# Optimization experiments

Measured on AMD Instinct MI355X. Metric: run time of the kernel, lower is better.

Reference implementation:

```python
import jax, jax.numpy as jnp
import numpy as np

N, F, H, K, E = 50000, 64, 64, 16, 800000
EXPONENT = 1.0  # module default; s = softmax(logits)**exponent, renormalized
EPS = 1e-15


def gcn_conv(x, W, b, src, dst, ew, n):
    """GCNConv: X' = D^{-1/2}(A+I)D^{-1/2} X W + b (symmetric norm, self-loops)."""
    h = x @ W  # [N,H] linear before propagation
    idx = jnp.arange(n)
    src_a = jnp.concatenate([src, idx])
    dst_a = jnp.concatenate([dst, idx])
    w_a = jnp.concatenate([ew, jnp.ones((n,), h.dtype)])
    deg = jax.ops.segment_sum(w_a, dst_a, num_segments=n)
    dinv = jnp.where(deg > 0, jax.lax.rsqrt(deg), 0.0)
    norm = dinv[src_a] * w_a * dinv[dst_a]          # [E+N]
    out = jax.ops.segment_sum(norm[:, None] * h[src_a], dst_a, num_segments=n)
    return out + b


def setup_inputs() -> dict:
    key = jax.random.key(0)
    ks = jax.random.split(key, 10)
    x = jax.random.normal(ks[0], (N, F), dtype=jnp.float32)
    edge_index = jax.random.randint(ks[1], (2, E), 0, N, dtype=jnp.int64)
    edge_weight = jax.random.uniform(ks[2], (E,), dtype=jnp.float32)
    W1 = jax.random.normal(ks[3], (F, H), dtype=jnp.float32) * (1.0 / np.sqrt(F))
    b1 = jnp.zeros((H,), jnp.float32)
    W2 = jax.random.normal(ks[4], (H, H), dtype=jnp.float32) * (1.0 / np.sqrt(H))
    b2 = jnp.zeros((H,), jnp.float32)
    Wp = jax.random.normal(ks[5], (H, K), dtype=jnp.float32) * (1.0 / np.sqrt(H))
    bp = jnp.zeros((K,), jnp.float32)
    return {"x": x, "edge_index": edge_index, "edge_weight": edge_weight,
            "W1": W1, "b1": b1, "W2": W2, "b2": b2, "Wp": Wp, "bp": bp}


def reference(x, edge_index, edge_weight, W1, b1, W2, b2, Wp, bp):
    src, dst = edge_index[0], edge_index[1]
    n = x.shape[0]
    k = Wp.shape[1]
    # stacked GCN + SELU
    h = jax.nn.selu(gcn_conv(x, W1, b1, src, dst, edge_weight, n))
    h = jax.nn.selu(gcn_conv(h, W2, b2, src, dst, edge_weight, n))
    # DMoN soft assignment
    s = jax.nn.softmax(h @ Wp + bp, axis=-1)          # [N,K]
    s = s ** EXPONENT
    s = s / s.sum(-1, keepdims=True)
    # pooled features: SELU(S^T X)
    out = jax.nn.selu(s.T @ h)                        # [K,H]
    # pooled adjacency: S^T A S computed over the edge list
    out_adj = jnp.einsum('ek,ec->kc', s[src] * edge_weight[:, None], s[dst])
    # spectral (modularity) loss
    d = jax.ops.segment_sum(edge_weight, src, num_segments=n)  # degrees
    two_m = edge_weight.sum()
    ca = s.T @ d                                      # [K]
    spectral_loss = -(jnp.trace(out_adj) - (ca @ ca) / two_m) / two_m
    # orthogonality loss
    ss = s.T @ s
    i_k = jnp.eye(k, dtype=s.dtype)
    ortho_loss = jnp.linalg.norm(ss / jnp.linalg.norm(ss) - i_k / jnp.sqrt(jnp.float32(k)))
    # cluster-size loss
    cluster_loss = jnp.linalg.norm(s.sum(0)) / n * jnp.sqrt(jnp.float32(k)) - 1.0
    # post-process pooled adjacency: zero diag, symmetric degree normalization
    adj = out_adj * (1.0 - i_k)
    dd = jnp.sqrt(adj.sum(-1))[:, None] + EPS
    adj = adj / dd / dd.T
    return s[None], out[None], adj[None], spectral_loss, ortho_loss, cluster_loss
```

## Files before the change

kernel.cpp:

```cpp
#include <hip/hip_runtime.h>
#include <hip/hip_bf16.h>

typedef __hip_bfloat16 bf16;
typedef long long i64t;

__device__ __forceinline__ float b2f(bf16 x) { return __bfloat162float(x); }
__device__ __forceinline__ bf16 f2b(float x) { return __float2bfloat16(x); }

__device__ __forceinline__ float loadF(const void* p, int isbf, long long i) {
    return isbf ? b2f(((const bf16*)p)[i]) : ((const float*)p)[i];
}
__device__ __forceinline__ int loadI(const void* p, int is64, long long i) {
    return is64 ? (int)((const i64t*)p)[i] : ((const int*)p)[i];
}
__device__ __forceinline__ void storeO(void* p, int isbf, long long i, float v) {
    if (isbf) ((bf16*)p)[i] = f2b(v);
    else ((float*)p)[i] = v;
}

#define SELU_ALPHA 1.6732632423543772f
#define SELU_SCALE 1.0507009873554805f
__device__ __forceinline__ float selu_f(float x) {
    return SELU_SCALE * (x > 0.f ? x : SELU_ALPHA * (expf(x) - 1.f));
}

__device__ __forceinline__ void atomAddF(float* p, float v) { unsafeAtomicAdd(p, v); }

__device__ __forceinline__ int pk_src(unsigned p) { return (int)(p >> 16); }
__device__ __forceinline__ float pk_w(unsigned p) { return __uint_as_float(p << 16); }

#define RED_STY 0
#define RED_OADJ 1024
#define RED_SS 1280
#define RED_CA 1536
#define RED_CS 1552
#define RED_2M 1568

#define NB_OADJ 1024
#define NB_ST 1024

#define CH 2048
#define NBK 256
#define BW 256

__global__ void k_probe(const void* W1, const void* eidx, int* flags) {
    __shared__ int sc[2];
    if (threadIdx.x == 0) { sc[0] = 0; sc[1] = 0; }
    __syncthreads();
    const unsigned* w = (const unsigned*)W1;
    int c0 = 0;
    for (int i = threadIdx.x; i < 2048; i += 256) {
        unsigned lo = w[i] & 0xFFFFu;
        unsigned e = (lo >> 7) & 0xFFu;
        if (e == 0u || (e >= 0x60u && e <= 0x8Fu)) c0++;
    }
    const unsigned* iw = (const unsigned*)eidx;
    int c1 = 0;
    for (int i = threadIdx.x; i < 2048; i += 256)
        if (iw[2 * i + 1] == 0u) c1++;
    atomicAdd(&sc[0], c0);
    atomicAdd(&sc[1], c1);
    __syncthreads();
    if (threadIdx.x == 0) {
        flags[0] = sc[0] > 1200 ? 1 : 0;
        flags[1] = sc[1] > 1024 ? 1 : 0;
    }
}

__global__ void k_bhist(const void* __restrict__ eidx, const int* __restrict__ flags,
                        int* __restrict__ gbcnt, int E) {
    __shared__ int cnt[NBK];
    int t = threadIdx.x;
    cnt[t] = 0;
    __syncthreads();
    int fi = flags[1];
    int base = blockIdx.x * CH;
    int m = min(CH, E - base);
    for (int k = t; k < m; k += 256) {
        int d = loadI(eidx, fi, (long long)E + base + k);
        atomicAdd(&cnt[d >> 8], 1);
    }
    __syncthreads();
    if (cnt[t]) atomicAdd(&gbcnt[t], cnt[t]);
}

__global__ void k_scanB(const int* __restrict__ gbcnt, int* __restrict__ gofs,
                        int* __restrict__ bbase) {
    __shared__ int part[NBK];
    int t = threadIdx.x;
    int c = gbcnt[t];
    part[t] = c;
    __syncthreads();
    for (int off = 1; off < NBK; off <<= 1) {
        int v = (t >= off) ? part[t - off] : 0;
        __syncthreads();
        part[t] += v;
        __syncthreads();
    }
    int ex = t ? part[t - 1] : 0;
    bbase[t] = ex;
    gofs[t] = ex;
    if (t == NBK - 1) bbase[NBK] = part[NBK - 1];
}

__global__ void k_bscatter(const void* __restrict__ eidx, const void* __restrict__ ew,
                           const int* __restrict__ flags, int* __restrict__ gofs,
                           uint2* __restrict__ tmp, int E) {
    __shared__ int cnt[NBK];
    __shared__ int binStart[NBK];
    __shared__ int bofs[NBK];
    __shared__ int runBase[NBK];
    __shared__ int sc[NBK];
    __shared__ uint2 staged[CH];
    int t = threadIdx.x;
    cnt[t] = 0;
    __syncthreads();
    int fb = flags[0], fi = flags[1];
    int base = blockIdx.x * CH;
    int m = min(CH, E - base);
    unsigned es[8], ed[8];
#pragma unroll
    for (int u = 0; u < 8; u++) {
        int k = t + u * 256;
        if (k < m) {
            int s = loadI(eidx, fi, base + k);
            int d = loadI(eidx, fi, (long long)E + base + k);
            float w = loadF(ew, fb, base + k);
            unsigned wb = (__float_as_uint(w) + 0x8000u) >> 16;
            es[u] = ((unsigned)s << 16) | wb;
            ed[u] = (unsigned)d;
            atomicAdd(&cnt[d >> 8], 1);
        } else {
            ed[u] = 0xFFFFFFFFu;
        }
    }
    __syncthreads();
    sc[t] = cnt[t];
    __syncthreads();
    for (int off = 1; off < NBK; off <<= 1) {
        int v = (t >= off) ? sc[t - off] : 0;
        __syncthreads();
        sc[t] += v;
        __syncthreads();
    }
    int ex = t ? sc[t - 1] : 0;
    binStart[t] = ex;
    bofs[t] = ex;
    __syncthreads();
#pragma unroll
    for (int u = 0; u < 8; u++) {
        if (ed[u] != 0xFFFFFFFFu) {
            int b = (int)(ed[u] >> 8);
            int li = atomicAdd(&bofs[b], 1);
            staged[li] = make_uint2(es[u], ed[u]);
        }
    }
    int c = cnt[t];
    __syncthreads();
    runBase[t] = c ? atomicAdd(&gofs[t], c) : 0;
    __syncthreads();
    for (int i = t; i < m; i += 256) {
        uint2 e = staged[i];
        int b = (int)(e.y >> 8);
        tmp[(long long)runBase[b] + (i - binStart[b])] = e;
    }
}

__global__ void k_build(const uint2* __restrict__ tmp, const int* __restrict__ bbase,
                        int* __restrict__ rowptr, unsigned* __restrict__ srcW,
                        float* __restrict__ dinv, float* __restrict__ two_m,
                        int n, int E) {
    __shared__ int cnt[BW];
    __shared__ int nofs[BW];
    __shared__ float wsum[BW];
    __shared__ int inc[BW];
    int b = blockIdx.x;
    int t = threadIdx.x;
    int n0 = b << 8;
    int nn = min(BW, n - n0);
    cnt[t] = 0;
    wsum[t] = 0.f;
    __syncthreads();
    int lo = bbase[b], hi = bbase[b + 1];
    for (int i = lo + t; i < hi; i += 256) {
        uint2 e = tmp[i];
        int dlo = (int)e.y - n0;
        atomicAdd(&cnt[dlo], 1);
        atomicAdd(&wsum[dlo], pk_w(e.x));
    }
    __syncthreads();
    inc[t] = cnt[t];
    __syncthreads();
    for (int off = 1; off < BW; off <<= 1) {
        int v = (t >= off) ? inc[t - off] : 0;
        __syncthreads();
        inc[t] += v;
        __syncthreads();
    }
    if (t < nn) {
        int ex = t ? inc[t - 1] : 0;
        rowptr[n0 + t] = lo + ex;
        nofs[t] = lo + ex;
        dinv[n0 + t] = rsqrtf(wsum[t] + 1.f);
    }
    if (b == (int)gridDim.x - 1 && t == 0) rowptr[n] = E;
    {
        float v = (t < nn) ? wsum[t] : 0.f;
        __shared__ float part[4];
        for (int mm = 32; mm; mm >>= 1) v += __shfl_down(v, mm, 64);
        int wid = t >> 6, lane = t & 63;
        if (lane == 0) part[wid] = v;
        __syncthreads();
        if (t == 0) atomAddF(two_m, part[0] + part[1] + part[2] + part[3]);
    }
    __syncthreads();
    for (int i = lo + t; i < hi; i += 256) {
        uint2 e = tmp[i];
        int dlo = (int)e.y - n0;
        int pos = atomicAdd(&nofs[dlo], 1);
        srcW[pos] = e.x;
    }
}

__global__ void k_gemm64(const void* __restrict__ in, int in_tag,
                         const void* __restrict__ W, const int* __restrict__ flags,
                         bf16* __restrict__ out, int n) {
    __shared__ float Wl[4096];
    __shared__ float Rl[2048];
    int t = threadIdx.x;
    int fb = flags[0];
    int inbf = in_tag ? fb : 0;
    for (int idx = t; idx < 4096; idx += 256) Wl[idx] = loadF(W, fb, idx);
    int r0 = blockIdx.x * 32;
    for (int idx = t; idx < 2048; idx += 256) {
        int rl = idx >> 6, k = idx & 63;
        int r = r0 + rl;
        Rl[idx] = (r < n) ? loadF(in, inbf, (long long)r * 64 + k) : 0.f;
    }
    __syncthreads();
    int rl = t >> 6, c = t & 63;
    float acc[8];
#pragma unroll
    for (int u = 0; u < 8; u++) acc[u] = 0.f;
    for (int k = 0; k < 64; k++) {
        float wv = Wl[k * 64 + c];
#pragma unroll
        for (int u = 0; u < 8; u++) acc[u] += Rl[(rl + (u << 2)) * 64 + k] * wv;
    }
#pragma unroll
    for (int u = 0; u < 8; u++) {
        int r = r0 + rl + (u << 2);
        if (r < n) out[(long long)r * 64 + c] = f2b(acc[u]);
    }
}

__global__ void k_prop_csr(const int* __restrict__ rowptr, const unsigned* __restrict__ srcW,
                           const float* __restrict__ dinv, const bf16* __restrict__ hin,
                           const void* __restrict__ b, const int* __restrict__ flags,
                           float* __restrict__ out, int n) {
    int t = threadIdx.x;
    int node = blockIdx.x * 4 + (t >> 6);
    if (node >= n) return;
    int l = t & 63;
    int q = l >> 4;
    int k = l & 15;
    int fb = flags[0];
    int i0 = rowptr[node], i1 = rowptr[node + 1];
    float di = dinv[node];
    float a0 = 0.f, a1 = 0.f, a2 = 0.f, a3 = 0.f;
    for (int base = i0; base < i1; base += 64) {
        int idx = base + l;
        unsigned p = (idx < i1) ? srcW[idx] : 0u;
        float cw = pk_w(p) * dinv[pk_src(p)];
        int m = i1 - base;
        if (m > 64) m = 64;
        for (int j = 0; j < m; j += 4) {
            unsigned pe = (unsigned)__shfl((int)p, j + q, 64);
            float c = __shfl(cw, j + q, 64);
            int s = (int)(pe >> 16);
            uint2 hv = *(const uint2*)(hin + ((long long)s << 6) + (k << 2));
            a0 += c * __uint_as_float(hv.x << 16);
            a1 += c * __uint_as_float(hv.x & 0xFFFF0000u);
            a2 += c * __uint_as_float(hv.y << 16);
            a3 += c * __uint_as_float(hv.y & 0xFFFF0000u);
        }
    }
    a0 += __shfl_xor(a0, 16, 64); a0 += __shfl_xor(a0, 32, 64);
    a1 += __shfl_xor(a1, 16, 64); a1 += __shfl_xor(a1, 32, 64);
    a2 += __shfl_xor(a2, 16, 64); a2 += __shfl_xor(a2, 32, 64);
    a3 += __shfl_xor(a3, 16, 64); a3 += __shfl_xor(a3, 32, 64);
    if (q == 0) {
        uint2 hv = *(const uint2*)(hin + ((long long)node << 6) + (k << 2));
        float dd = di * di;
        float v0 = di * a0 + dd * __uint_as_float(hv.x << 16) + loadF(b, fb, 4 * k);
        float v1 = di * a1 + dd * __uint_as_float(hv.x & 0xFFFF0000u) + loadF(b, fb, 4 * k + 1);
        float v2 = di * a2 + dd * __uint_as_float(hv.y << 16) + loadF(b, fb, 4 * k + 2);
        float v3 = di * a3 + dd * __uint_as_float(hv.y & 0xFFFF0000u) + loadF(b, fb, 4 * k + 3);
        float4 r = make_float4(selu_f(v0), selu_f(v1), selu_f(v2), selu_f(v3));
        *(float4*)(out + ((long long)node << 6) + (k << 2)) = r;
    }
}

__global__ void k_softmax(const float* __restrict__ y, const void* __restrict__ Wp,
                          const void* __restrict__ bp, const int* __restrict__ flags,
                          float* __restrict__ sbuf, void* __restrict__ sout, int n) {
    __shared__ float Wl[1024];
    __shared__ float bl[16];
    __shared__ float yl[1024];
    int t = threadIdx.x;
    int fb = flags[0];
    for (int idx = t; idx < 1024; idx += 256) Wl[idx] = loadF(Wp, fb, idx);
    if (t < 16) bl[t] = loadF(bp, fb, t);
    int g0 = blockIdx.x * 16;
    for (int idx = t; idx < 1024; idx += 256) {
        int nl = idx >> 6, f = idx & 63;
        int g = g0 + nl;
        yl[idx] = (g < n) ? y[(long long)g * 64 + f] : 0.f;
    }
    __syncthreads();
    int nl = t >> 4, k = t & 15;
    int g = g0 + nl;
    float logit = bl[k];
#pragma unroll
    for (int jj = 0; jj < 64; jj++) logit += yl[nl * 64 + jj] * Wl[jj * 16 + k];
    float mx = logit;
    for (int m = 8; m; m >>= 1) mx = fmaxf(mx, __shfl_xor(mx, m, 16));
    float e = expf(logit - mx);
    float sum = e;
    for (int m = 8; m; m >>= 1) sum += __shfl_xor(sum, m, 16);
    float sv = e / sum;
    if (g < n) {
        sbuf[(long long)g * 16 + k] = sv;
        storeO(sout, fb, (long long)g * 16 + k, sv);
    }
}

__global__ void k_stats(const float* __restrict__ s, const float* __restrict__ y,
                        float* __restrict__ scratch, int n) {
    __shared__ float lsty[1024];
    __shared__ float lss[256];
    int t = threadIdx.x;
    int w = t >> 6, f = t & 63;
    for (int i = t; i < 1024; i += 256) lsty[i] = 0.f;
    lss[t] = 0.f;
    __syncthreads();
    int chunk = (n + NB_ST - 1) / NB_ST;
    int start = min(blockIdx.x * chunk, n);
    int end = min(start + chunk, n);
    int q = (chunk + 3) >> 2;
    int n0 = min(start + w * q, end);
    int n1 = min(n0 + q, end);
    float acc[16], accss[16];
#pragma unroll
    for (int k = 0; k < 16; k++) { acc[k] = 0.f; accss[k] = 0.f; }
    for (int node = n0; node < n1; node++) {
        float yv = y[(long long)node * 64 + f];
        float sv = (f < 16) ? s[(long long)node * 16 + f] : 0.f;
#pragma unroll
        for (int k = 0; k < 16; k++) {
            float sk = __shfl(sv, k, 64);
            acc[k] += sk * yv;
            accss[k] += sk * sv;
        }
    }
#pragma unroll
    for (int k = 0; k < 16; k++) atomicAdd(&lsty[k * 64 + f], acc[k]);
    if (f < 16) {
#pragma unroll
        for (int k = 0; k < 16; k++) atomicAdd(&lss[k * 16 + f], accss[k]);
    }
    __syncthreads();
    float* dst = scratch + (long long)blockIdx.x * 1280;
    for (int i = t; i < 1024; i += 256) dst[i] = lsty[i];
    dst[1024 + t] = lss[t];
}

__global__ void k_stats_reduce(const float* __restrict__ scratch, float* __restrict__ red) {
    int o = blockIdx.x;
    int t = threadIdx.x;
    float sum = 0.f;
#pragma unroll
    for (int k = 0; k < NB_ST / 256; k++)
        sum += scratch[(long long)(t + 256 * k) * 1280 + o];
    __shared__ float part[4];
    for (int m = 32; m; m >>= 1) sum += __shfl_down(sum, m, 64);
    int wid = t >> 6, lane = t & 63;
    if (lane == 0) part[wid] = sum;
    __syncthreads();
    if (t == 0) {
        float v = part[0] + part[1] + part[2] + part[3];
        if (o < 1024) red[RED_STY + o] = v;
        else red[RED_SS + o - 1024] = v;
    }
}

__global__ void k_outadj_csr(const int* __restrict__ rowptr, const unsigned* __restrict__ srcW,
                             const float* __restrict__ s, float* __restrict__ scratch,
                             int n) {
    __shared__ float lacc[256];
    __shared__ float sca[16];
    __shared__ float scs[16];
    int t = threadIdx.x;
    int wv = t >> 6;
    int l = t & 63;
    int q = l >> 4;
    int j = l & 15;
    lacc[t] = 0.f;
    if (t < 16) { sca[t] = 0.f; scs[t] = 0.f; }
    __syncthreads();
    float acc[16];
#pragma unroll
    for (int r = 0; r < 16; r++) acc[r] = 0.f;
    float catot = 0.f, cstot = 0.f;
    for (int node = blockIdx.x * 4 + wv; node < n; node += gridDim.x * 4) {
        int i0 = rowptr[node], i1 = rowptr[node + 1];
        float tv = 0.f;
        for (int base = i0; base < i1; base += 64) {
            int idx = base + l;
            unsigned p = (idx < i1) ? srcW[idx] : 0u;
            float wl = pk_w(p);
            int m = i1 - base;
            if (m > 64) m = 64;
            for (int jj = 0; jj < m; jj += 4) {
                unsigned pe = (unsigned)__shfl((int)p, jj + q, 64);
                float w = __shfl(wl, jj + q, 64);
                int sidx = (int)(pe >> 16);
                tv += w * s[(long long)sidx * 16 + j];
            }
        }
        tv += __shfl_xor(tv, 16, 64);
        tv += __shfl_xor(tv, 32, 64);
        float sj = s[(long long)node * 16 + j];
        if (q == 0) {
            catot += tv;
            cstot += sj;
        }
#pragma unroll
        for (int r = 0; r < 16; r++) acc[r] += __shfl(tv, r, 16) * sj;
    }
    if (q == 0) {
#pragma unroll
        for (int r = 0; r < 16; r++) atomicAdd(&lacc[r * 16 + j], acc[r]);
        atomicAdd(&sca[j], catot);
        atomicAdd(&scs[j], cstot);
    }
    __syncthreads();
    float* dstp = scratch + (long long)blockIdx.x * 288;
    dstp[t] = lacc[t];
    if (t < 16) {
        dstp[256 + t] = sca[t];
        dstp[272 + t] = scs[t];
    }
}

__global__ void k_oadj_reduce(const float* __restrict__ scratch, float* __restrict__ red) {
    int o = blockIdx.x;
    int t = threadIdx.x;
    float sum = 0.f;
#pragma unroll
    for (int k = 0; k < NB_OADJ / 256; k++)
        sum += scratch[(long long)(t + 256 * k) * 288 + o];
    __shared__ float part[4];
    for (int m = 32; m; m >>= 1) sum += __shfl_down(sum, m, 64);
    int wid = t >> 6, lane = t & 63;
    if (lane == 0) part[wid] = sum;
    __syncthreads();
    if (t == 0) {
        float v = part[0] + part[1] + part[2] + part[3];
        if (o < 256) red[RED_OADJ + o] = v;
        else if (o < 272) red[RED_CA + o - 256] = v;
        else red[RED_CS + o - 272] = v;
    }
}

__device__ float blockReduceSum256(float v) {
    __shared__ float part[4];
    for (int m = 32; m; m >>= 1) v += __shfl_down(v, m, 64);
    int wid = threadIdx.x >> 6, lane = threadIdx.x & 63;
    if (lane == 0) part[wid] = v;
    __syncthreads();
    v = part[0] + part[1] + part[2] + part[3];
    __syncthreads();
    return v;
}

__global__ void k_finalize(const float* __restrict__ red, void* __restrict__ out,
                           const int* __restrict__ flags, int n_nodes, int base) {
    int t = threadIdx.x;
    int fb = flags[0];
    for (int idx = t; idx < 1024; idx += 256)
        storeO(out, fb, base + idx, selu_f(red[RED_STY + idx]));
    int i = t >> 4, j = t & 15;
    float ss_t = red[RED_SS + t];
    float oadj_t = red[RED_OADJ + t];
    float two_m = red[RED_2M];

    float norm_ss = sqrtf(blockReduceSum256(ss_t * ss_t));
    float diff = ss_t / norm_ss - ((i == j) ? 0.25f : 0.f);
    float ortho = sqrtf(blockReduceSum256(diff * diff));
    float trace = blockReduceSum256((i == j) ? oadj_t : 0.f);
    float ca_t = (t < 16) ? red[RED_CA + t] : 0.f;
    float cad = blockReduceSum256(ca_t * ca_t);
    float spectral = -(trace - cad / two_m) / two_m;
    float cs_t = (t < 16) ? red[RED_CS + t] : 0.f;
    float cluster = sqrtf(blockReduceSum256(cs_t * cs_t)) / (float)n_nodes * 4.f - 1.f;

    float a = (i == j) ? 0.f : oadj_t;
    float rs = a;
    for (int m = 8; m; m >>= 1) rs += __shfl_xor(rs, m, 16);
    __shared__ float ddl[16];
    float dd_i = sqrtf(rs) + 1e-15f;
    if (j == 0) ddl[i] = dd_i;
    __syncthreads();
    float aout = a / (dd_i * ddl[j]);
    storeO(out, fb, base + 1024 + t, aout);
    if (t == 0) {
        storeO(out, fb, base + 1280, spectral);
        storeO(out, fb, base + 1281, ortho);
        storeO(out, fb, base + 1282, cluster);
    }
}

extern "C" void kernel_launch(void* const* d_in, const int* in_sizes, int n_in,
                              void* d_out, int out_size, void* d_ws, size_t ws_size,
                              hipStream_t stream) {
    const void* x = d_in[0];
    const void* eidx = d_in[1];
    const void* ew = d_in[2];
    const void* W1 = d_in[3];
    const void* b1 = d_in[4];
    const void* W2 = d_in[5];
    const void* b2 = d_in[6];
    const void* Wp = d_in[7];
    const void* bp = d_in[8];

    const int N = in_sizes[0] / 64;
    const int E = in_sizes[2];

    float* ws = (float*)d_ws;
    float* B = ws;
    float* hbf_f = B + (size_t)N * 64;
    bf16* hbf = (bf16*)hbf_f;
    float* sbuf = hbf_f;
    float* dinv = hbf_f + (size_t)N * 32;
    int* rowptr = (int*)(dinv + N);
    float* red = (float*)(rowptr + (N + 1));
    int* flags = (int*)(red + 2048);
    int* gbcnt = flags + 2;
    int* gofs = gbcnt + NBK;
    int* bbase = gofs + NBK;
    size_t off_ints = (size_t)((bbase + NBK + 1) - (int*)ws);
    off_ints = (off_ints + 1) & ~(size_t)1;
    unsigned* srcW = (unsigned*)((int*)ws + off_ints);
    size_t off2 = off_ints + (size_t)E;
    off2 = (off2 + 1) & ~(size_t)1;
    uint2* tmp = (uint2*)((int*)ws + off2);
    float* scratch = (float*)tmp;

    hipMemsetAsync(gbcnt, 0, sizeof(int) * NBK, stream);
    hipMemsetAsync(red, 0, sizeof(float) * 2048 + 2 * sizeof(int), stream);

    int nbA = (E + CH - 1) / CH;
    int nbK = (N + BW - 1) / BW;
    k_probe<<<1, 256, 0, stream>>>(W1, eidx, flags);
    k_bhist<<<nbA, 256, 0, stream>>>(eidx, flags, gbcnt, E);
    k_scanB<<<1, 256, 0, stream>>>(gbcnt, gofs, bbase);
    k_bscatter<<<nbA, 256, 0, stream>>>(eidx, ew, flags, gofs, tmp, E);
    k_build<<<nbK, 256, 0, stream>>>(tmp, bbase, rowptr, srcW, dinv, red + RED_2M, N, E);

    k_gemm64<<<(N + 31) / 32, 256, 0, stream>>>(x, 1, W1, flags, hbf, N);
    k_prop_csr<<<(N + 3) / 4, 256, 0, stream>>>(rowptr, srcW, dinv, hbf, b1, flags, B, N);
    k_gemm64<<<(N + 31) / 32, 256, 0, stream>>>(B, 0, W2, flags, hbf, N);
    k_prop_csr<<<(N + 3) / 4, 256, 0, stream>>>(rowptr, srcW, dinv, hbf, b2, flags, B, N);

    k_softmax<<<(N + 15) / 16, 256, 0, stream>>>(B, Wp, bp, flags, sbuf, d_out, N);
    k_stats<<<NB_ST, 256, 0, stream>>>(sbuf, B, scratch, N);
    k_stats_reduce<<<1280, 256, 0, stream>>>(scratch, red);
    k_outadj_csr<<<NB_OADJ, 256, 0, stream>>>(rowptr, srcW, sbuf, scratch, N);
    k_oadj_reduce<<<288, 256, 0, stream>>>(scratch, red);
    k_finalize<<<1, 256, 0, stream>>>(red, d_out, flags, N, N * 16);
}
```

Measured before the change: 367.9 us.

## Fuse probe into histogram, stats into softmax, and merge final reductions

Dtype probing moves into every block of the edge histogram kernel, which removes a separate launch. The S^T·Y and S^T·S partial sums are now computed inside the softmax kernel from its shared-memory tiles, so the separate stats pass over y and s goes away. The two reduction kernels are merged into one launch and the two memsets become one. The trade-off is that per-block scratch grows to about 3125 blocks × 1280 floats, which makes the combined reduction read far more data than the old 1024-block version.

```diff
diff --git a/kernel.cpp b/kernel.cpp
--- a/kernel.cpp
+++ b/kernel.cpp
@@ -37,43 +37,37 @@
 #define RED_2M 1568
 
 #define NB_OADJ 1024
-#define NB_ST 1024
-
 #define CH 2048
 #define NBK 256
 #define BW 256
 
-__global__ void k_probe(const void* W1, const void* eidx, int* flags) {
-    __shared__ int sc[2];
-    if (threadIdx.x == 0) { sc[0] = 0; sc[1] = 0; }
+__global__ void k_bhist(const void* __restrict__ W1, const void* __restrict__ eidx,
+                        int* __restrict__ flags, int* __restrict__ gbcnt, int E) {
+    __shared__ int cnt[NBK];
+    __shared__ int sc2[2];
+    int t = threadIdx.x;
+    cnt[t] = 0;
+    if (t < 2) sc2[t] = 0;
     __syncthreads();
     const unsigned* w = (const unsigned*)W1;
     int c0 = 0;
-    for (int i = threadIdx.x; i < 2048; i += 256) {
+    for (int i = t; i < 2048; i += 256) {
         unsigned lo = w[i] & 0xFFFFu;
         unsigned e = (lo >> 7) & 0xFFu;
         if (e == 0u || (e >= 0x60u && e <= 0x8Fu)) c0++;
     }
     const unsigned* iw = (const unsigned*)eidx;
     int c1 = 0;
-    for (int i = threadIdx.x; i < 2048; i += 256)
+    for (int i = t; i < 2048; i += 256)
         if (iw[2 * i + 1] == 0u) c1++;
-    atomicAdd(&sc[0], c0);
-    atomicAdd(&sc[1], c1);
-    __syncthreads();
-    if (threadIdx.x == 0) {
-        flags[0] = sc[0] > 1200 ? 1 : 0;
-        flags[1] = sc[1] > 1024 ? 1 : 0;
-    }
-}
-
-__global__ void k_bhist(const void* __restrict__ eidx, const int* __restrict__ flags,
-                        int* __restrict__ gbcnt, int E) {
-    __shared__ int cnt[NBK];
-    int t = threadIdx.x;
-    cnt[t] = 0;
-    __syncthreads();
-    int fi = flags[1];
+    atomicAdd(&sc2[0], c0);
+    atomicAdd(&sc2[1], c1);
+    __syncthreads();
+    int fi = sc2[1] > 1024 ? 1 : 0;
+    if (blockIdx.x == 0 && t == 0) {
+        flags[0] = sc2[0] > 1200 ? 1 : 0;
+        flags[1] = fi;
+    }
     int base = blockIdx.x * CH;
     int m = min(CH, E - base);
     for (int k = t; k < m; k += 256) {
@@ -303,10 +297,12 @@
 
 __global__ void k_softmax(const float* __restrict__ y, const void* __restrict__ Wp,
                           const void* __restrict__ bp, const int* __restrict__ flags,
-                          float* __restrict__ sbuf, void* __restrict__ sout, int n) {
+                          float* __restrict__ sbuf, void* __restrict__ sout,
+                          float* __restrict__ scratch, int n) {
     __shared__ float Wl[1024];
     __shared__ float bl[16];
     __shared__ float yl[1024];
+    __shared__ float sl[256];
     int t = threadIdx.x;
     int fb = flags[0];
     for (int idx = t; idx < 1024; idx += 256) Wl[idx] = loadF(Wp, fb, idx);
@@ -329,68 +325,36 @@
     float sum = e;
     for (int m = 8; m; m >>= 1) sum += __shfl_xor(sum, m, 16);
     float sv = e / sum;
+    sl[nl * 16 + k] = (g < n) ? sv : 0.f;
     if (g < n) {
         sbuf[(long long)g * 16 + k] = sv;
         storeO(sout, fb, (long long)g * 16 + k, sv);
     }
-}
-
-__global__ void k_stats(const float* __restrict__ s, const float* __restrict__ y,
-                        float* __restrict__ scratch, int n) {
-    __shared__ float lsty[1024];
-    __shared__ float lss[256];
-    int t = threadIdx.x;
-    int w = t >> 6, f = t & 63;
-    for (int i = t; i < 1024; i += 256) lsty[i] = 0.f;
-    lss[t] = 0.f;
-    __syncthreads();
-    int chunk = (n + NB_ST - 1) / NB_ST;
-    int start = min(blockIdx.x * chunk, n);
-    int end = min(start + chunk, n);
-    int q = (chunk + 3) >> 2;
-    int n0 = min(start + w * q, end);
-    int n1 = min(n0 + q, end);
-    float acc[16], accss[16];
-#pragma unroll
-    for (int k = 0; k < 16; k++) { acc[k] = 0.f; accss[k] = 0.f; }
-    for (int node = n0; node < n1; node++) {
-        float yv = y[(long long)node * 64 + f];
-        float sv = (f < 16) ? s[(long long)node * 16 + f] : 0.f;
-#pragma unroll
-        for (int k = 0; k < 16; k++) {
-            float sk = __shfl(sv, k, 64);
-            acc[k] += sk * yv;
-            accss[k] += sk * sv;
-        }
-    }
-#pragma unroll
-    for (int k = 0; k < 16; k++) atomicAdd(&lsty[k * 64 + f], acc[k]);
-    if (f < 16) {
-#pragma unroll
-        for (int k = 0; k < 16; k++) atomicAdd(&lss[k * 16 + f], accss[k]);
-    }
     __syncthreads();
     float* dst = scratch + (long long)blockIdx.x * 1280;
-    for (int i = t; i < 1024; i += 256) dst[i] = lsty[i];
-    dst[1024 + t] = lss[t];
-}
-
-__global__ void k_stats_reduce(const float* __restrict__ scratch, float* __restrict__ red) {
-    int o = blockIdx.x;
-    int t = threadIdx.x;
-    float sum = 0.f;
-#pragma unroll
-    for (int k = 0; k < NB_ST / 256; k++)
-        sum += scratch[(long long)(t + 256 * k) * 1280 + o];
-    __shared__ float part[4];
-    for (int m = 32; m; m >>= 1) sum += __shfl_down(sum, m, 64);
-    int wid = t >> 6, lane = t & 63;
-    if (lane == 0) part[wid] = sum;
-    __syncthreads();
-    if (t == 0) {
-        float v = part[0] + part[1] + part[2] + part[3];
-        if (o < 1024) red[RED_STY + o] = v;
-        else red[RED_SS + o - 1024] = v;
+    {
+        int k4 = t >> 6, f = t & 63;
+        float a0 = 0.f, a1 = 0.f, a2 = 0.f, a3 = 0.f;
+#pragma unroll
+        for (int node = 0; node < 16; node++) {
+            float yv = yl[node * 64 + f];
+            const float* sp = sl + node * 16;
+            a0 += sp[k4] * yv;
+            a1 += sp[k4 + 4] * yv;
+            a2 += sp[k4 + 8] * yv;
+            a3 += sp[k4 + 12] * yv;
+        }
+        dst[k4 * 64 + f] = a0;
+        dst[(k4 + 4) * 64 + f] = a1;
+        dst[(k4 + 8) * 64 + f] = a2;
+        dst[(k4 + 12) * 64 + f] = a3;
+    }
+    {
+        int i = t >> 4, j = t & 15;
+        float ssa = 0.f;
+#pragma unroll
+        for (int node = 0; node < 16; node++) ssa += sl[node * 16 + i] * sl[node * 16 + j];
+        dst[1024 + t] = ssa;
     }
 }
 
@@ -453,13 +417,17 @@
     }
 }
 
-__global__ void k_oadj_reduce(const float* __restrict__ scratch, float* __restrict__ red) {
+__global__ void k_reduce_all(const float* __restrict__ sscr, const float* __restrict__ oscr,
+                             float* __restrict__ red, int nbS) {
     int o = blockIdx.x;
     int t = threadIdx.x;
     float sum = 0.f;
-#pragma unroll
-    for (int k = 0; k < NB_OADJ / 256; k++)
-        sum += scratch[(long long)(t + 256 * k) * 288 + o];
+    if (o < 1280) {
+        for (int b = t; b < nbS; b += 256) sum += sscr[(long long)b * 1280 + o];
+    } else {
+        int oo = o - 1280;
+        for (int b = t; b < NB_OADJ; b += 256) sum += oscr[(long long)b * 288 + oo];
+    }
     __shared__ float part[4];
     for (int m = 32; m; m >>= 1) sum += __shfl_down(sum, m, 64);
     int wid = t >> 6, lane = t & 63;
@@ -467,9 +435,14 @@
     __syncthreads();
     if (t == 0) {
         float v = part[0] + part[1] + part[2] + part[3];
-        if (o < 256) red[RED_OADJ + o] = v;
-        else if (o < 272) red[RED_CA + o - 256] = v;
-        else red[RED_CS + o - 272] = v;
+        if (o < 1024) red[RED_STY + o] = v;
+        else if (o < 1280) red[RED_SS + o - 1024] = v;
+        else {
+            int oo = o - 1280;
+            if (oo < 256) red[RED_OADJ + oo] = v;
+            else if (oo < 272) red[RED_CA + oo - 256] = v;
+            else red[RED_CS + oo - 272] = v;
+        }
     }
 }
 
@@ -545,9 +518,9 @@
     float* dinv = hbf_f + (size_t)N * 32;
     int* rowptr = (int*)(dinv + N);
     float* red = (float*)(rowptr + (N + 1));
-    int* flags = (int*)(red + 2048);
-    int* gbcnt = flags + 2;
-    int* gofs = gbcnt + NBK;
+    int* gbcnt = (int*)(red + 2048);
+    int* flags = gbcnt + NBK;
+    int* gofs = flags + 2;
     int* bbase = gofs + NBK;
     size_t off_ints = (size_t)((bbase + NBK + 1) - (int*)ws);
     off_ints = (off_ints + 1) & ~(size_t)1;
@@ -555,15 +528,15 @@
     size_t off2 = off_ints + (size_t)E;
     off2 = (off2 + 1) & ~(size_t)1;
     uint2* tmp = (uint2*)((int*)ws + off2);
-    float* scratch = (float*)tmp;
-
-    hipMemsetAsync(gbcnt, 0, sizeof(int) * NBK, stream);
-    hipMemsetAsync(red, 0, sizeof(float) * 2048 + 2 * sizeof(int), stream);
+    float* sscr = (float*)tmp;
+    int nbS = (N + 15) / 16;
+    float* oscr = sscr + (size_t)nbS * 1280;
+
+    hipMemsetAsync(red, 0, sizeof(float) * (2048 + NBK), stream);
 
     int nbA = (E + CH - 1) / CH;
     int nbK = (N + BW - 1) / BW;
-    k_probe<<<1, 256, 0, stream>>>(W1, eidx, flags);
-    k_bhist<<<nbA, 256, 0, stream>>>(eidx, flags, gbcnt, E);
+    k_bhist<<<nbA, 256, 0, stream>>>(W1, eidx, flags, gbcnt, E);
     k_scanB<<<1, 256, 0, stream>>>(gbcnt, gofs, bbase);
     k_bscatter<<<nbA, 256, 0, stream>>>(eidx, ew, flags, gofs, tmp, E);
     k_build<<<nbK, 256, 0, stream>>>(tmp, bbase, rowptr, srcW, dinv, red + RED_2M, N, E);
@@ -573,10 +546,8 @@
     k_gemm64<<<(N + 31) / 32, 256, 0, stream>>>(B, 0, W2, flags, hbf, N);
     k_prop_csr<<<(N + 3) / 4, 256, 0, stream>>>(rowptr, srcW, dinv, hbf, b2, flags, B, N);
 
-    k_softmax<<<(N + 15) / 16, 256, 0, stream>>>(B, Wp, bp, flags, sbuf, d_out, N);
-    k_stats<<<NB_ST, 256, 0, stream>>>(sbuf, B, scratch, N);
-    k_stats_reduce<<<1280, 256, 0, stream>>>(scratch, red);
-    k_outadj_csr<<<NB_OADJ, 256, 0, stream>>>(rowptr, srcW, sbuf, scratch, N);
-    k_oadj_reduce<<<288, 256, 0, stream>>>(scratch, red);
+    k_softmax<<<nbS, 256, 0, stream>>>(B, Wp, bp, flags, sbuf, d_out, sscr, N);
+    k_outadj_csr<<<NB_OADJ, 256, 0, stream>>>(rowptr, srcW, sbuf, oscr, N);
+    k_reduce_all<<<1280 + 288, 256, 0, stream>>>(sscr, oscr, red, nbS);
     k_finalize<<<1, 256, 0, stream>>>(red, d_out, flags, N, N * 16);
 }
```

After: 342.9 us. 1.07x faster.
